# Optimization experiments

Measured on AMD Instinct MI355X. Metric: run time of the kernel, lower is better.

## Reference

```python
import jax, jax.numpy as jnp
import numpy as np

B, S, H, NH = 8, 1024, 1024, 16
DH = H // NH


def setup_inputs() -> dict:
    key = jax.random.key(0)
    ks = jax.random.split(key, 16)
    inp = {
        'v': jax.random.normal(ks[0], (B, S, H), jnp.float32),
        'k': jax.random.normal(ks[1], (B, S, H), jnp.float32),
        'q': jax.random.normal(ks[2], (B, S, H), jnp.float32),
        'r': jax.random.normal(ks[3], (B, S, H), jnp.float32),
        'mask': jax.random.randint(ks[4], (B, 1, 1, S), 0, 2).astype(jnp.bool_),
    }
    scale = 1.0 / np.sqrt(H)
    names = ['Wv', 'Wk', 'Wq', 'Wr', 'Wm']
    for i, n in enumerate(names):
        inp[n] = jax.random.normal(ks[5 + i], (H, H), jnp.float32) * scale
        inp['b' + n[1:]] = jnp.zeros((H,), jnp.float32)
    return inp


def _heads(x, W, b):
    # torch Linear: x @ W.T + b, then split heads -> [B, NH, S, DH]
    y = jnp.einsum('bsh,oh->bso', x, W) + b
    return y.reshape(B, S, NH, DH).transpose(0, 2, 1, 3)


def reference(v, k, q, r, mask, Wv, bv, Wk, bk, Wq, bq, Wr, br, Wm, bm):
    vh = _heads(v, Wv, bv)
    kh = _heads(k, Wk, bk)
    qh = _heads(q, Wq, bq)
    rh = _heads(r, Wr, br)
    # relation-augmented scores: (QK^T + RK^T) / sqrt(d_k)
    scores = jnp.einsum('bhqd,bhkd->bhqk', qh + rh, kh) / jnp.sqrt(jnp.asarray(DH, qh.dtype))
    scores = jnp.where(mask, jnp.asarray(-1e9, scores.dtype), scores)
    att = jax.nn.softmax(scores, axis=-1)  # dropout = identity in eval
    out = jnp.einsum('bhqk,bhkd->bhqd', att, vh)
    out = out.transpose(0, 2, 1, 3).reshape(B, S, H)
    return jnp.einsum('bsh,oh->bso', out, Wm) + bm
```

## Files before the change

### kernel.cpp

```cpp
#include <hip/hip_runtime.h>
#include <hip/hip_bf16.h>
#include <stdint.h>

typedef __attribute__((ext_vector_type(4))) float f32x4;
typedef __attribute__((ext_vector_type(8))) short s16x8;
typedef __attribute__((ext_vector_type(4))) short s16x4;
typedef __attribute__((ext_vector_type(4))) int i32x4;

typedef const __attribute__((address_space(1))) unsigned glb_u32;
typedef __attribute__((address_space(3))) unsigned lds_u32;

#define DEVI __device__ __forceinline__

DEVI short f2b(float f) {
    union { float f; unsigned u; } v; v.f = f;
    unsigned r = v.u + 0x7fffu + ((v.u >> 16) & 1u);
    return (short)(r >> 16);
}

DEVI float vexp2(float x) {
    float r;
    asm("v_exp_f32 %0, %1" : "=v"(r) : "v"(x));
    return r;
}

DEVI float vmax3(float a, float b, float c) {
    float d;
    asm("v_max3_f32 %0, %1, %2, %3" : "=v"(d) : "v"(a), "v"(b), "v"(c));
    return d;
}

DEVI unsigned cvtpk(float lo, float hi) {
    unsigned d;
    asm("v_cvt_pk_bf16_f32 %0, %1, %2" : "=v"(d) : "v"(lo), "v"(hi));
    return d;
}

DEVI s16x8 pack8(const f32x4& a, const f32x4& b) {
    union { unsigned u[4]; s16x8 v; } w;
    w.u[0] = cvtpk(a[0], a[1]);
    w.u[1] = cvtpk(a[2], a[3]);
    w.u[2] = cvtpk(b[0], b[1]);
    w.u[3] = cvtpk(b[2], b[3]);
    return w.v;
}

#define QSCL 0.18033688011112042f
#define MASKV -1.4426950408889634e9f

struct Ptr5 { const float* p[5]; };
struct Ptr4 { const float* p[4]; };

__global__ __launch_bounds__(256) void cvtW(Ptr5 src, short* __restrict__ dst) {
    const float* s = src.p[blockIdx.y];
    short* d = dst + (size_t)blockIdx.y * (1024u * 1024u);
    int i = (blockIdx.x * 256 + threadIdx.x) * 8;
    f32x4 a = *(const f32x4*)(s + i);
    f32x4 b = *(const f32x4*)(s + i + 4);
    s16x8 o;
#pragma unroll
    for (int j = 0; j < 4; ++j) { o[j] = f2b(a[j]); o[4 + j] = f2b(b[j]); }
    *(s16x8*)(d + i) = o;
}

__global__ __launch_bounds__(256) void cvtA(Ptr4 src, short* __restrict__ dst) {
    const float* s = src.p[blockIdx.y];
    short* d = dst + (size_t)blockIdx.y * (8u * 1024u * 1024u);
    int i = (blockIdx.x * 256 + threadIdx.x) * 8;
    f32x4 a = *(const f32x4*)(s + i);
    f32x4 b = *(const f32x4*)(s + i + 4);
    s16x8 o;
#pragma unroll
    for (int j = 0; j < 4; ++j) { o[j] = f2b(a[j]); o[4 + j] = f2b(b[j]); }
    *(s16x8*)(d + i) = o;
}

template<int AF32, int OUTMODE, int TWO>
__global__ __launch_bounds__(256) void gemm_nt(
    const void* __restrict__ A0_, const void* __restrict__ A1_,
    const short* __restrict__ W0, const short* __restrict__ W1,
    const float* __restrict__ b0, const float* __restrict__ b1,
    void* __restrict__ C_)
{
    constexpr int K = 1024, N = 1024;
    const int tid = threadIdx.x;
    const int lane = tid & 63, wid = tid >> 6;
    const int wm = wid >> 1, wn = wid & 1;
    const int r = lane & 15, g = lane >> 4;

    const int bid = blockIdx.x;
    const int logical = (bid & 7) * 64 + (bid >> 3);
    const int n0 = (logical & 7) * 128, m0 = (logical >> 3) * 128;

    __shared__ alignas(16) short As[2][128 * 32];
    __shared__ alignas(16) short Ws[2][128 * 32];

    auto stage_async = [&](int buf, int kt) {
        int kk = kt * 32;
        const short* Ap = (const short*)A0_; const short* Wp = W0;
        if (TWO && kk >= 1024) { Ap = (const short*)A1_; Wp = W1; kk &= 1023; }
#pragma unroll
        for (int i = 0; i < 2; ++i) {
            int row = wid * 32 + i * 16 + (lane >> 2);
            const short* ga = Ap + (size_t)(m0 + row) * K + kk + (lane & 3) * 8;
            const short* gw = Wp + (size_t)(n0 + row) * K + kk + (lane & 3) * 8;
            __builtin_amdgcn_global_load_lds((glb_u32*)ga,
                (lds_u32*)&As[buf][(wid * 32 + i * 16) * 32], 16, 0, 0);
            __builtin_amdgcn_global_load_lds((glb_u32*)gw,
                (lds_u32*)&Ws[buf][(wid * 32 + i * 16) * 32], 16, 0, 0);
        }
    };

    const int srow = tid >> 1, shalf = tid & 1;
    f32x4 a0g, a1g, a2g, a3g;
    s16x8 wg0, wg1;
    auto load_regs = [&](int kt) {
        int kk = kt * 32;
        const short* wp = W0 + (size_t)(n0 + srow) * K + kk + shalf * 16;
        wg0 = *(const s16x8*)wp;
        wg1 = *(const s16x8*)(wp + 8);
        const float* ap = (const float*)A0_ + (size_t)(m0 + srow) * K + kk + shalf * 16;
        a0g = *(const f32x4*)ap;       a1g = *(const f32x4*)(ap + 4);
        a2g = *(const f32x4*)(ap + 8); a3g = *(const f32x4*)(ap + 12);
    };
    auto store_lds = [&](int buf) {
        s16x8 s0, s1;
#pragma unroll
        for (int j = 0; j < 4; ++j) {
            s0[j] = f2b(a0g[j]); s0[4 + j] = f2b(a1g[j]);
            s1[j] = f2b(a2g[j]); s1[4 + j] = f2b(a3g[j]);
        }
        char* ab = (char*)As[buf];
        *(s16x8*)(ab + srow * 64 + shalf * 32) = s0;
        *(s16x8*)(ab + srow * 64 + shalf * 32 + 16) = s1;
        char* wb = (char*)Ws[buf];
        *(s16x8*)(wb + srow * 64 + shalf * 32) = wg0;
        *(s16x8*)(wb + srow * 64 + shalf * 32 + 16) = wg1;
    };

    f32x4 z = {0.f, 0.f, 0.f, 0.f};
    f32x4 acc[4][4];
#pragma unroll
    for (int i = 0; i < 4; ++i)
#pragma unroll
        for (int j = 0; j < 4; ++j) acc[i][j] = z;

    auto compute = [&](int buf) {
        s16x8 af[4], bfr[4];
#pragma unroll
        for (int f = 0; f < 4; ++f) {
            af[f]  = *(const s16x8*)&As[buf][(wm * 64 + f * 16 + r) * 32 + g * 8];
            bfr[f] = *(const s16x8*)&Ws[buf][(wn * 64 + f * 16 + r) * 32 + g * 8];
        }
#pragma unroll
        for (int i = 0; i < 4; ++i)
#pragma unroll
            for (int j = 0; j < 4; ++j)
                acc[i][j] = __builtin_amdgcn_mfma_f32_16x16x32_bf16(af[i], bfr[j], acc[i][j], 0, 0, 0);
    };

    constexpr int NK = TWO ? 64 : 32;
    if constexpr (AF32) { load_regs(0); store_lds(0); }
    else stage_async(0, 0);
    __syncthreads();
    int buf = 0;
    for (int kt = 0; kt < NK; ++kt) {
        if (kt + 1 < NK) {
            if constexpr (AF32) load_regs(kt + 1);
            else stage_async(buf ^ 1, kt + 1);
        }
        compute(buf);
        if (AF32 && kt + 1 < NK) store_lds(buf ^ 1);
        __syncthreads();
        buf ^= 1;
    }

#pragma unroll
    for (int j = 0; j < 4; ++j) {
        int col = n0 + wn * 64 + j * 16 + r;
        float bb = b0[col];
        if (TWO) bb += b1[col];
#pragma unroll
        for (int i = 0; i < 4; ++i) {
            int rowb = m0 + wm * 64 + i * 16 + g * 4;
            if constexpr (OUTMODE == 2) {
                int bb_ = rowb >> 10, tok = rowb & 1023;
                int tokp = (tok & ~31) | (((tok >> 2) & 3) << 3) | (((tok >> 4) & 1) << 2);
                short* dst = (short*)C_ + ((size_t)(bb_ * 16 + (col >> 6))) * 65536
                           + (size_t)(col & 63) * 1024 + tokp;
                s16x4 o;
#pragma unroll
                for (int q = 0; q < 4; ++q) o[q] = f2b(acc[i][j][q] + bb);
                *(s16x4*)dst = o;
            } else {
#pragma unroll
                for (int q = 0; q < 4; ++q) {
                    float val = acc[i][j][q] + bb;
                    if constexpr (OUTMODE == 1)
                        ((float*)C_)[(size_t)(rowb + q) * N + col] = val;
                    else
                        ((short*)C_)[(size_t)(rowb + q) * N + col] = f2b(val);
                }
            }
        }
    }
}

__global__ __launch_bounds__(256) void attn_fwd(
    const short* __restrict__ qrh, const short* __restrict__ kh,
    const short* __restrict__ vT, const int* __restrict__ mask,
    short* __restrict__ outp)
{
    const int bh = blockIdx.x;
    const int b = bh >> 4, h = bh & 15;
    const int qt = blockIdx.y;
    const int tid = threadIdx.x, lane = tid & 63, wid = tid >> 6;
    const int r = lane & 15, g = lane >> 4;

    __shared__ alignas(16) short Ks[64 * 64];
    __shared__ alignas(16) short Vs[64 * 64];
    __shared__ alignas(16) float mb[1024];

    {
        i32x4 mi = *(const i32x4*)(mask + b * 1024 + tid * 4);
        f32x4 mv;
#pragma unroll
        for (int j = 0; j < 4; ++j) mv[j] = mi[j] ? MASKV : 0.f;
        *(f32x4*)&mb[tid * 4] = mv;
    }

    const int q0 = qt * 128 + wid * 32;
    const short* qbA = qrh + (size_t)(b * 1024 + q0 + r) * 1024 + h * 64;
    const short* qbB = qbA + 16 * 1024;
    s16x8 qA0 = *(const s16x8*)(qbA + g * 8);
    s16x8 qA1 = *(const s16x8*)(qbA + 32 + g * 8);
    s16x8 qB0 = *(const s16x8*)(qbB + g * 8);
    s16x8 qB1 = *(const s16x8*)(qbB + 32 + g * 8);

    f32x4 z = {0.f, 0.f, 0.f, 0.f};
    f32x4 oA[4], oB[4];
#pragma unroll
    for (int i = 0; i < 4; ++i) { oA[i] = z; oB[i] = z; }
    float mA = -1e30f, mB = -1e30f, lA = 0.f, lB = 0.f;

    const int srow = tid >> 2, sq = tid & 3;
    const short* kg = kh + (size_t)(b * 1024 + srow) * 1024 + h * 64 + sq * 16;
    const short* vg = vT + ((size_t)(b * 16 + h)) * 65536 + (size_t)srow * 1024 + sq * 16;
    const int p0s = (sq * 2) ^ (srow & 7), p1s = (sq * 2 + 1) ^ (srow & 7);

    s16x8 kr0, kr1, vr0, vr1;
    auto stage_load = [&](int t) {
        const short* kp = kg + (size_t)(t * 64) * 1024;
        kr0 = *(const s16x8*)kp; kr1 = *(const s16x8*)(kp + 8);
        const short* vp = vg + t * 64;
        vr0 = *(const s16x8*)vp; vr1 = *(const s16x8*)(vp + 8);
    };
    auto stage_write = [&]() {
        char* kb2 = (char*)Ks;
        *(s16x8*)(kb2 + srow * 128 + p0s * 16) = kr0;
        *(s16x8*)(kb2 + srow * 128 + p1s * 16) = kr1;
        char* vb2 = (char*)Vs;
        *(s16x8*)(vb2 + srow * 128 + p0s * 16) = vr0;
        *(s16x8*)(vb2 + srow * 128 + p1s * 16) = vr1;
    };

    stage_load(0);
    for (int t = 0; t < 16; ++t) {
        if (t) __syncthreads();
        stage_write();
        __syncthreads();
        if (t < 15) stage_load(t + 1);

        f32x4 pA[4], pB[4];
        float tmA = -3e38f, tmB = -3e38f;
        char* kb2 = (char*)Ks;
#pragma unroll
        for (int fn = 0; fn < 4; ++fn) {
            int row = fn * 16 + r;
            s16x8 kfa = *(const s16x8*)(kb2 + row * 128 + ((g ^ (row & 7)) << 4));
            s16x8 kfb = *(const s16x8*)(kb2 + row * 128 + (((4 + g) ^ (row & 7)) << 4));
            f32x4 cA = __builtin_amdgcn_mfma_f32_16x16x32_bf16(kfa, qA0, z, 0, 0, 0);
            cA = __builtin_amdgcn_mfma_f32_16x16x32_bf16(kfb, qA1, cA, 0, 0, 0);
            f32x4 cB = __builtin_amdgcn_mfma_f32_16x16x32_bf16(kfa, qB0, z, 0, 0, 0);
            cB = __builtin_amdgcn_mfma_f32_16x16x32_bf16(kfb, qB1, cB, 0, 0, 0);
            f32x4 mv = *(const f32x4*)&mb[t * 64 + fn * 16 + g * 4];
#pragma unroll
            for (int qi = 0; qi < 4; ++qi) {
                pA[fn][qi] = cA[qi] * QSCL + mv[qi];
                pB[fn][qi] = cB[qi] * QSCL + mv[qi];
            }
            tmA = vmax3(tmA, pA[fn][0], pA[fn][1]);
            tmA = vmax3(tmA, pA[fn][2], pA[fn][3]);
            tmB = vmax3(tmB, pB[fn][0], pB[fn][1]);
            tmB = vmax3(tmB, pB[fn][2], pB[fn][3]);
        }
        tmA = fmaxf(tmA, __shfl_xor(tmA, 16)); tmA = fmaxf(tmA, __shfl_xor(tmA, 32));
        tmB = fmaxf(tmB, __shfl_xor(tmB, 16)); tmB = fmaxf(tmB, __shfl_xor(tmB, 32));

        float mnA = fmaxf(mA, tmA), mnB = fmaxf(mB, tmB);
        float cA_ = vexp2(mA - mnA), cB_ = vexp2(mB - mnB);
        mA = mnA; mB = mnB;
        float tsA = 0.f, tsB = 0.f;
#pragma unroll
        for (int fn = 0; fn < 4; ++fn)
#pragma unroll
            for (int qi = 0; qi < 4; ++qi) {
                float eA = vexp2(pA[fn][qi] - mA); pA[fn][qi] = eA; tsA += eA;
                float eB = vexp2(pB[fn][qi] - mB); pB[fn][qi] = eB; tsB += eB;
            }
        tsA += __shfl_xor(tsA, 16); tsA += __shfl_xor(tsA, 32);
        tsB += __shfl_xor(tsB, 16); tsB += __shfl_xor(tsB, 32);
        lA = lA * cA_ + tsA; lB = lB * cB_ + tsB;
#pragma unroll
        for (int df = 0; df < 4; ++df)
#pragma unroll
            for (int qi = 0; qi < 4; ++qi) { oA[df][qi] *= cA_; oB[df][qi] *= cB_; }

        char* vb2 = (char*)Vs;
#pragma unroll
        for (int ks = 0; ks < 2; ++ks) {
            s16x8 pbA = pack8(pA[2 * ks], pA[2 * ks + 1]);
            s16x8 pbB = pack8(pB[2 * ks], pB[2 * ks + 1]);
#pragma unroll
            for (int df = 0; df < 4; ++df) {
                int row = df * 16 + r;
                int slot = (ks * 4 + g) ^ (row & 7);
                s16x8 vf = *(const s16x8*)(vb2 + row * 128 + (slot << 4));
                oA[df] = __builtin_amdgcn_mfma_f32_16x16x32_bf16(vf, pbA, oA[df], 0, 0, 0);
                oB[df] = __builtin_amdgcn_mfma_f32_16x16x32_bf16(vf, pbB, oB[df], 0, 0, 0);
            }
        }
    }

    float ivA = 1.f / lA, ivB = 1.f / lB;
#pragma unroll
    for (int df = 0; df < 4; ++df) {
        s16x4 oa, ob;
#pragma unroll
        for (int qi = 0; qi < 4; ++qi) {
            oa[qi] = f2b(oA[df][qi] * ivA);
            ob[qi] = f2b(oB[df][qi] * ivB);
        }
        *(s16x4*)&outp[(size_t)(b * 1024 + q0 + r) * 1024 + h * 64 + df * 16 + g * 4] = oa;
        *(s16x4*)&outp[(size_t)(b * 1024 + q0 + 16 + r) * 1024 + h * 64 + df * 16 + g * 4] = ob;
    }
}

extern "C" void kernel_launch(void* const* d_in, const int* in_sizes, int n_in,
                              void* d_out, int out_size, void* d_ws, size_t ws_size,
                              hipStream_t stream) {
    const float* v  = (const float*)d_in[0];
    const float* k  = (const float*)d_in[1];
    const float* q  = (const float*)d_in[2];
    const float* rr = (const float*)d_in[3];
    const int* mask = (const int*)d_in[4];
    const float* Wv = (const float*)d_in[5];  const float* bv = (const float*)d_in[6];
    const float* Wk = (const float*)d_in[7];  const float* bk = (const float*)d_in[8];
    const float* Wq = (const float*)d_in[9];  const float* bq = (const float*)d_in[10];
    const float* Wr = (const float*)d_in[11]; const float* br = (const float*)d_in[12];
    const float* Wm = (const float*)d_in[13]; const float* bm = (const float*)d_in[14];

    const size_t MB = 1048576u;
    const size_t NEED_FULL = 90u * MB;
    const size_t NEED_B    = 74u * MB;
    char* ws = (char*)d_ws;
    short* Wb = (short*)ws;

    Ptr5 p5;
    p5.p[0] = Wv; p5.p[1] = Wk; p5.p[2] = Wq; p5.p[3] = Wr; p5.p[4] = Wm;
    cvtW<<<dim3(512, 5), 256, 0, stream>>>(p5, Wb);

    const short* Wvb = Wb, *Wkb = Wb + 1048576u, *Wqb = Wb + 2097152u,
               *Wrb = Wb + 3145728u, *Wmb = Wb + 4194304u;
    dim3 gg(512);

    if (ws_size >= NEED_FULL) {
        short* vb  = (short*)(ws + 10u * MB);
        short* kb  = vb + 8388608u;
        short* qb  = kb + 8388608u;
        short* rb  = qb + 8388608u;
        short* vtb = rb + 8388608u;
        short* khb = vb;
        short* qrb = kb;
        short* att = qb;

        Ptr4 p4; p4.p[0] = v; p4.p[1] = k; p4.p[2] = q; p4.p[3] = rr;
        cvtA<<<dim3(4096, 4), 256, 0, stream>>>(p4, vb);

        gemm_nt<0, 2, 0><<<gg, 256, 0, stream>>>(vb, nullptr, Wvb, nullptr, bv, nullptr, vtb);
        gemm_nt<0, 0, 0><<<gg, 256, 0, stream>>>(kb, nullptr, Wkb, nullptr, bk, nullptr, khb);
        gemm_nt<0, 0, 1><<<gg, 256, 0, stream>>>(qb, rb, Wqb, Wrb, bq, br, qrb);
        attn_fwd<<<dim3(128, 8), 256, 0, stream>>>(qrb, khb, vtb, mask, att);
        gemm_nt<0, 1, 0><<<gg, 256, 0, stream>>>(att, nullptr, Wmb, nullptr, bm, nullptr, (float*)d_out);
    } else if (ws_size >= NEED_B) {
        short* kb  = (short*)(ws + 10u * MB);
        short* qb  = kb + 8388608u;
        short* rb  = qb + 8388608u;
        short* qrb = rb + 8388608u;
        short* vtb = qb;
        short* khb = rb;
        short* att = kb;

        Ptr4 p4; p4.p[0] = k; p4.p[1] = q; p4.p[2] = rr; p4.p[3] = k;
        cvtA<<<dim3(4096, 3), 256, 0, stream>>>(p4, kb);

        gemm_nt<0, 0, 1><<<gg, 256, 0, stream>>>(qb, rb, Wqb, Wrb, bq, br, qrb);
        gemm_nt<1, 2, 0><<<gg, 256, 0, stream>>>(v, nullptr, Wvb, nullptr, bv, nullptr, vtb);
        gemm_nt<0, 0, 0><<<gg, 256, 0, stream>>>(kb, nullptr, Wkb, nullptr, bk, nullptr, khb);
        attn_fwd<<<dim3(128, 8), 256, 0, stream>>>(qrb, khb, vtb, mask, att);
        gemm_nt<0, 1, 0><<<gg, 256, 0, stream>>>(att, nullptr, Wmb, nullptr, bm, nullptr, (float*)d_out);
    }
}
```

Baseline: 242.6 us.

## Double-buffer K/V tiles via direct global-to-LDS loads in attention

```diff
diff --git a/kernel.cpp b/kernel.cpp
--- a/kernel.cpp
+++ b/kernel.cpp
@@ -217,8 +217,8 @@
     const int tid = threadIdx.x, lane = tid & 63, wid = tid >> 6;
     const int r = lane & 15, g = lane >> 4;
 
-    __shared__ alignas(16) short Ks[64 * 64];
-    __shared__ alignas(16) short Vs[64 * 64];
+    __shared__ alignas(16) short Ks[2][64 * 64];
+    __shared__ alignas(16) short Vs[2][64 * 64];
     __shared__ alignas(16) float mb[1024];
 
     {
@@ -243,42 +243,56 @@
     for (int i = 0; i < 4; ++i) { oA[i] = z; oB[i] = z; }
     float mA = -1e30f, mB = -1e30f, lA = 0.f, lB = 0.f;
 
-    const int srow = tid >> 2, sq = tid & 3;
-    const short* kg = kh + (size_t)(b * 1024 + srow) * 1024 + h * 64 + sq * 16;
-    const short* vg = vT + ((size_t)(b * 16 + h)) * 65536 + (size_t)srow * 1024 + sq * 16;
-    const int p0s = (sq * 2) ^ (srow & 7), p1s = (sq * 2 + 1) ^ (srow & 7);
-
-    s16x8 kr0, kr1, vr0, vr1;
-    auto stage_load = [&](int t) {
-        const short* kp = kg + (size_t)(t * 64) * 1024;
-        kr0 = *(const s16x8*)kp; kr1 = *(const s16x8*)(kp + 8);
-        const short* vp = vg + t * 64;
-        vr0 = *(const s16x8*)vp; vr1 = *(const s16x8*)(vp + 8);
+    const int lrow = lane >> 3;
+    const int lq = (lane & 7) ^ (lrow & 7);
+    const short* kgp[2];
+    const short* vgp[2];
+#pragma unroll
+    for (int i = 0; i < 2; ++i) {
+        int R0 = wid * 16 + i * 8;
+        kgp[i] = kh + (size_t)(b * 1024 + R0 + lrow) * 1024 + h * 64 + lq * 8;
+        vgp[i] = vT + ((size_t)(b * 16 + h)) * 65536 + (size_t)(R0 + lrow) * 1024 + lq * 8;
+    }
+    auto stage = [&](int t, int bufi) {
+#pragma unroll
+        for (int i = 0; i < 2; ++i) {
+            __builtin_amdgcn_global_load_lds((glb_u32*)(kgp[i] + (size_t)t * 65536),
+                (lds_u32*)&Ks[bufi][(wid * 16 + i * 8) * 64], 16, 0, 0);
+            __builtin_amdgcn_global_load_lds((glb_u32*)(vgp[i] + t * 64),
+                (lds_u32*)&Vs[bufi][(wid * 16 + i * 8) * 64], 16, 0, 0);
+        }
     };
-    auto stage_write = [&]() {
-        char* kb2 = (char*)Ks;
-        *(s16x8*)(kb2 + srow * 128 + p0s * 16) = kr0;
-        *(s16x8*)(kb2 + srow * 128 + p1s * 16) = kr1;
-        char* vb2 = (char*)Vs;
-        *(s16x8*)(vb2 + srow * 128 + p0s * 16) = vr0;
-        *(s16x8*)(vb2 + srow * 128 + p1s * 16) = vr1;
-    };
-
-    stage_load(0);
+
+    int koA[4], koB[4], vo[8];
+#pragma unroll
+    for (int fn = 0; fn < 4; ++fn) {
+        int row = fn * 16 + r;
+        koA[fn] = row * 128 + ((g ^ (row & 7)) << 4);
+        koB[fn] = row * 128 + (((4 + g) ^ (row & 7)) << 4);
+    }
+#pragma unroll
+    for (int ks = 0; ks < 2; ++ks)
+#pragma unroll
+        for (int df = 0; df < 4; ++df) {
+            int row = df * 16 + r;
+            vo[ks * 4 + df] = row * 128 + (((ks * 4 + g) ^ (row & 7)) << 4);
+        }
+
+    stage(0, 0);
+    __syncthreads();
+    int buf = 0;
     for (int t = 0; t < 16; ++t) {
-        if (t) __syncthreads();
-        stage_write();
-        __syncthreads();
-        if (t < 15) stage_load(t + 1);
+        if (t < 15) stage(t + 1, buf ^ 1);
+
+        const char* kb2 = (const char*)Ks[buf];
+        const char* vb2 = (const char*)Vs[buf];
 
         f32x4 pA[4], pB[4];
         float tmA = -3e38f, tmB = -3e38f;
-        char* kb2 = (char*)Ks;
 #pragma unroll
         for (int fn = 0; fn < 4; ++fn) {
-            int row = fn * 16 + r;
-            s16x8 kfa = *(const s16x8*)(kb2 + row * 128 + ((g ^ (row & 7)) << 4));
-            s16x8 kfb = *(const s16x8*)(kb2 + row * 128 + (((4 + g) ^ (row & 7)) << 4));
+            s16x8 kfa = *(const s16x8*)(kb2 + koA[fn]);
+            s16x8 kfb = *(const s16x8*)(kb2 + koB[fn]);
             f32x4 cA = __builtin_amdgcn_mfma_f32_16x16x32_bf16(kfa, qA0, z, 0, 0, 0);
             cA = __builtin_amdgcn_mfma_f32_16x16x32_bf16(kfb, qA1, cA, 0, 0, 0);
             f32x4 cB = __builtin_amdgcn_mfma_f32_16x16x32_bf16(kfa, qB0, z, 0, 0, 0);
@@ -316,20 +330,20 @@
 #pragma unroll
             for (int qi = 0; qi < 4; ++qi) { oA[df][qi] *= cA_; oB[df][qi] *= cB_; }
 
-        char* vb2 = (char*)Vs;
 #pragma unroll
         for (int ks = 0; ks < 2; ++ks) {
             s16x8 pbA = pack8(pA[2 * ks], pA[2 * ks + 1]);
             s16x8 pbB = pack8(pB[2 * ks], pB[2 * ks + 1]);
 #pragma unroll
             for (int df = 0; df < 4; ++df) {
-                int row = df * 16 + r;
-                int slot = (ks * 4 + g) ^ (row & 7);
-                s16x8 vf = *(const s16x8*)(vb2 + row * 128 + (slot << 4));
+                s16x8 vf = *(const s16x8*)(vb2 + vo[ks * 4 + df]);
                 oA[df] = __builtin_amdgcn_mfma_f32_16x16x32_bf16(vf, pbA, oA[df], 0, 0, 0);
                 oB[df] = __builtin_amdgcn_mfma_f32_16x16x32_bf16(vf, pbB, oB[df], 0, 0, 0);
             }
         }
+
+        __syncthreads();
+        buf ^= 1;
     }
 
     float ivA = 1.f / lA, ivB = 1.f / lB;
```

Measured after the change: 246.8 us. Within noise of the previous version (+1.7%).
